# Kernel optimization log

Measured on AMD Instinct MI355X. Metric: run time of the kernel, lower is better.

The kernel has to match this reference:

```python
import jax, jax.numpy as jnp
import numpy as np

N_NODES = 87381  # complete 4-ary tree of depth 9: (4**9 - 1) / 3
VOCAB = 32000
D_IN = 256
M_DIM = 256


def setup_inputs() -> dict:
    key = jax.random.key(0)
    ks = jax.random.split(key, 10)
    w = lambda k, s: jax.random.normal(k, s, dtype=jnp.float32) * 0.05
    return {
        "tokens": jax.random.randint(ks[0], (N_NODES,), 0, VOCAB),
        "branching": 4,
        "emb": w(ks[1], (VOCAB, D_IN)),
        "Wioux": w(ks[2], (D_IN, 3 * M_DIM)),
        "bioux": w(ks[3], (3 * M_DIM,)),
        "Wiouh": w(ks[4], (M_DIM, 3 * M_DIM)),
        "biouh": w(ks[5], (3 * M_DIM,)),
        "Wfx": w(ks[6], (D_IN, M_DIM)),
        "bfx": w(ks[7], (M_DIM,)),
        "Wfh": w(ks[8], (M_DIM, M_DIM)),
        "bfh": w(ks[9], (M_DIM,)),
    }


def _levels(n, b):
    # BFS level boundaries (start, size) for a complete b-ary tree with n nodes
    out, start, size = [], 0, 1
    while start < n:
        out.append((start, min(size, n - start)))
        start += size
        size *= b
    return out


def reference(tokens, branching, emb, Wioux, bioux, Wiouh, biouh, Wfx, bfx, Wfh, bfh):
    N = tokens.shape[0]
    b = int(branching)
    M = Wfh.shape[0]
    x = emb[tokens]                       # [N, D_IN] per-node inputs
    xiou = x @ Wioux + bioux              # [N, 3M] precomputed input gate terms
    xf = x @ Wfx + bfx                    # [N, M]
    h = jnp.zeros((N, M), x.dtype)
    c = jnp.zeros((N, M), x.dtype)
    for (s, sz) in reversed(_levels(N, b)):  # leaves -> root
        idx = jnp.arange(s, s + sz)
        child = idx[:, None] * b + 1 + jnp.arange(b)[None, :]   # [sz, b]
        valid = (child < N)[..., None].astype(x.dtype)          # [sz, b, 1]
        ci = jnp.where(child < N, child, 0)
        ch = h[ci] * valid                                      # [sz, b, M]
        cc = c[ci] * valid
        iou = xiou[idx] + ch.sum(axis=1) @ Wiouh + biouh        # [sz, 3M]
        i, o, u = jnp.split(iou, 3, axis=1)
        i, o, u = jax.nn.sigmoid(i), jax.nn.sigmoid(o), jnp.tanh(u)
        f = jax.nn.sigmoid(ch @ Wfh + bfh + xf[idx][:, None, :])  # [sz, b, M]
        c_new = i * u + jnp.sum(f * cc * valid, axis=1)
        h_new = o * jnp.tanh(c_new)
        c = c.at[idx].set(c_new)
        h = h.at[idx].set(h_new)
    return h  # hidden state of every node; root state is h[0]
```

## Files before the change

kernel.cpp:

```cpp
#include <hip/hip_runtime.h>
#include <cstdint>
#include <cstddef>

typedef _Float16 f16;
typedef __attribute__((ext_vector_type(8))) _Float16 half8;
typedef __attribute__((ext_vector_type(4))) _Float16 half4;
typedef __attribute__((ext_vector_type(8))) short short8;
typedef __attribute__((ext_vector_type(4))) float floatx4;
typedef __attribute__((ext_vector_type(8))) float floatx8;

__device__ __forceinline__ float rcp_(float x) { return __builtin_amdgcn_rcpf(x); }
__device__ __forceinline__ float sigm(float x) { return rcp_(1.f + __expf(-x)); }
__device__ __forceinline__ float tanh_(float x) { return 1.f - 2.f * rcp_(1.f + __expf(2.f * x)); }

__device__ __forceinline__ short8 ld16_coh(const void* p) {
  unsigned long long lo = __hip_atomic_load((const unsigned long long*)p,
      __ATOMIC_RELAXED, __HIP_MEMORY_SCOPE_AGENT);
  unsigned long long hi = __hip_atomic_load((const unsigned long long*)p + 1,
      __ATOMIC_RELAXED, __HIP_MEMORY_SCOPE_AGENT);
  union { unsigned long long u[2]; short8 s; } v;
  v.u[0] = lo; v.u[1] = hi;
  return v.s;
}
__device__ __forceinline__ void st2_coh(f16* p, f16 x) {
  __hip_atomic_store((unsigned short*)p, __builtin_bit_cast(unsigned short, x),
                     __ATOMIC_RELAXED, __HIP_MEMORY_SCOPE_AGENT);
}

__global__ __launch_bounds__(256) void gemm128d(
    const f16* __restrict__ A0, const f16* __restrict__ B0, f16* __restrict__ C0,
    int ldc0, int nt0, int tiles0,
    const f16* __restrict__ A1, const f16* __restrict__ B1, f16* __restrict__ C1,
    int ldc1, int nt1)
{
  const f16* A; const f16* BT; f16* C; int ldc_, mi, ni;
  int bid = blockIdx.x;
  bid = (bid & 7) * ((int)gridDim.x >> 3) + (bid >> 3);
  if (bid < tiles0) { A = A0; BT = B0; C = C0; ldc_ = ldc0; mi = bid / nt0; ni = bid % nt0; }
  else { int r = bid - tiles0; A = A1; BT = B1; C = C1; ldc_ = ldc1; mi = r / nt1; ni = r % nt1; }
  const int m0 = mi * 128;
  const int n0 = ni * 128;

  __shared__ short lA[128 * 72];
  __shared__ short lB[128 * 72];
  const int t = threadIdx.x;
  const int wave = t >> 6;
  const int lane = t & 63;
  const int ln = lane & 15;
  const int quad = lane >> 4;
  const int wr = wave >> 1;
  const int wc = wave & 1;

  floatx4 acc[4][4];
#pragma unroll
  for (int i = 0; i < 4; ++i)
#pragma unroll
    for (int j = 0; j < 4; ++j) acc[i][j] = (floatx4){0.f, 0.f, 0.f, 0.f};

#pragma unroll
  for (int st = 0; st < 4; ++st) {
    const int k0 = st * 64;
#pragma unroll
    for (int i = 0; i < 4; ++i) {
      int chunk = t + 256 * i;
      int row = chunk >> 3;
      int cc = chunk & 7;
      *(short8*)&lA[row * 72 + cc * 8] =
          *(const short8*)(A + (size_t)(m0 + row) * 256 + k0 + cc * 8);
      *(short8*)&lB[row * 72 + cc * 8] =
          *(const short8*)(BT + (size_t)(n0 + row) * 256 + k0 + cc * 8);
    }
    __syncthreads();
#pragma unroll
    for (int ks = 0; ks < 2; ++ks) {
      const int kk = ks * 32 + quad * 8;
      half8 a[4], b[4];
#pragma unroll
      for (int rf = 0; rf < 4; ++rf)
        a[rf] = __builtin_bit_cast(half8,
            *(const short8*)&lA[(wr * 64 + rf * 16 + ln) * 72 + kk]);
#pragma unroll
      for (int cf = 0; cf < 4; ++cf)
        b[cf] = __builtin_bit_cast(half8,
            *(const short8*)&lB[(wc * 64 + cf * 16 + ln) * 72 + kk]);
#pragma unroll
      for (int rf = 0; rf < 4; ++rf)
#pragma unroll
        for (int cf = 0; cf < 4; ++cf)
          acc[rf][cf] = __builtin_amdgcn_mfma_f32_16x16x32_f16(
              a[rf], b[cf], acc[rf][cf], 0, 0, 0);
    }
    __syncthreads();
  }
#pragma unroll
  for (int rf = 0; rf < 4; ++rf)
#pragma unroll
    for (int cf = 0; cf < 4; ++cf)
#pragma unroll
      for (int r = 0; r < 4; ++r) {
        int row = m0 + wr * 64 + rf * 16 + quad * 4 + r;
        int col = n0 + wc * 64 + cf * 16 + ln;
        C[(size_t)row * ldc_ + col] = (f16)acc[rf][cf][r];
      }
}

__global__ __launch_bounds__(256) void prep(
    const float* __restrict__ emb, const float* __restrict__ Wioux,
    const float* __restrict__ Wfx, const float* __restrict__ Wiouh,
    const float* __restrict__ Wfh,
    f16* __restrict__ emb_h, f16* __restrict__ BTX,
    f16* __restrict__ WiouhT, f16* __restrict__ WfhT,
    int* __restrict__ ctr)
{
  int idx = blockIdx.x * 256 + threadIdx.x;
  if (idx < 8) ctr[idx] = 0;
  if (idx < 2048000) {
    floatx4 v = *(const floatx4*)(emb + 4 * (size_t)idx);
    half4 o;
#pragma unroll
    for (int j = 0; j < 4; ++j) o[j] = (f16)v[j];
    *(half4*)(emb_h + 4 * (size_t)idx) = o;
  } else if (idx < 2310144) {
    int r = idx - 2048000;
    int j = r >> 8, k = r & 255;
    BTX[r] = (f16)((j < 768) ? Wioux[(size_t)k * 768 + j]
                             : Wfx[(size_t)k * 256 + (j - 768)]);
  } else if (idx < 2506752) {
    int r = idx - 2310144;
    int j = r >> 8, k = r & 255;
    WiouhT[r] = (f16)Wiouh[(size_t)k * 768 + j];
  } else {
    int r = idx - 2506752;
    int j = r >> 8, k = r & 255;
    WfhT[r] = (f16)Wfh[(size_t)k * 256 + j];
  }
}

__global__ __launch_bounds__(256) void elem8(
    const int* __restrict__ tokens, const f16* __restrict__ TIOUF,
    const float* __restrict__ bioux, const float* __restrict__ biouh,
    f16* __restrict__ c16, float* __restrict__ h, f16* __restrict__ h16,
    f16* __restrict__ hsum16, int s, int sz, int s_up, int sz_up)
{
  __shared__ float hsh[8 * 260];
  const int t = threadIdx.x;
  const int nloc = t >> 5;
  const int d0 = (t & 31) * 8;
  const int base = s + 8 * blockIdx.x;
  const int node = base + nloc;
  const int lim = s + sz;

  if (node < lim) {
    const f16* ti = TIOUF + (size_t)tokens[node] * 1024;
    half8 t0 = *(const half8*)(ti + d0);
    half8 t1 = *(const half8*)(ti + 256 + d0);
    half8 t2 = *(const half8*)(ti + 512 + d0);
    floatx8 bi0 = *(const floatx8*)(bioux + d0) + *(const floatx8*)(biouh + d0);
    floatx8 bi1 = *(const floatx8*)(bioux + 256 + d0) + *(const floatx8*)(biouh + 256 + d0);
    floatx8 bi2 = *(const floatx8*)(bioux + 512 + d0) + *(const floatx8*)(biouh + 512 + d0);

    float cv[8];
#pragma unroll
    for (int j = 0; j < 8; ++j)
      cv[j] = sigm((float)t0[j] + bi0[j]) * tanh_((float)t2[j] + bi2[j]);

    half8 c8, h8;
    floatx8 hf;
#pragma unroll
    for (int j = 0; j < 8; ++j) {
      float hv = sigm((float)t1[j] + bi1[j]) * tanh_(cv[j]);
      c8[j] = (f16)cv[j];
      h8[j] = (f16)hv;
      hf[j] = hv;
    }
    *(half8*)(c16 + (size_t)node * 256 + d0) = c8;
    *(floatx8*)(h + (size_t)node * 256 + d0) = hf;
    *(half8*)(h16 + (size_t)node * 256 + d0) = h8;
    *(floatx8*)&hsh[nloc * 260 + d0] = hf;
  }
  __syncthreads();

  if (t < 64) {
    int p = t >> 5;
    int dd = (t & 31) * 8;
    int parent = ((base - 1) >> 2) + p;
    if (parent < s_up + sz_up) {
      floatx8 v = *(const floatx8*)&hsh[(4 * p + 0) * 260 + dd] +
                  *(const floatx8*)&hsh[(4 * p + 1) * 260 + dd] +
                  *(const floatx8*)&hsh[(4 * p + 2) * 260 + dd] +
                  *(const floatx8*)&hsh[(4 * p + 3) * 260 + dd];
      half8 o;
#pragma unroll
      for (int j = 0; j < 8; ++j) o[j] = (f16)v[j];
      *(half8*)(hsum16 + (size_t)(parent - s_up) * 256 + dd) = o;
    }
  }
}

template <bool COH>
__device__ __forceinline__ void do_tile(
    short* lA, short* lC,
    const int* __restrict__ tokens, const f16* __restrict__ TIOUF,
    const f16* __restrict__ WiouhT, const f16* __restrict__ WfhT,
    const float* __restrict__ bioux, const float* __restrict__ biouh,
    const float* __restrict__ bfx, const float* __restrict__ bfh,
    f16* __restrict__ c16, float* __restrict__ h, f16* __restrict__ h16,
    const f16* __restrict__ hsum_in, f16* __restrict__ hsum_out,
    int s, int sz, int sz_up, int pt, int pg)
{
  const int t = threadIdx.x;
  const int p0 = s + pt * 16;
  const int c0 = 4 * p0 + 1;

#pragma unroll
  for (int i = 0; i < 5; ++i) {
    int chunk = t + 512 * i;
    int row = chunk >> 5;
    int cc = chunk & 31;
    const f16* src = (row < 16)
        ? hsum_in + (size_t)(pt * 16 + row) * 256 + cc * 8
        : h16 + (size_t)(c0 + row - 16) * 256 + cc * 8;
    short8 v;
    if constexpr (COH) v = ld16_coh(src); else v = *(const short8*)src;
    *(short8*)&lA[row * 256 + (cc ^ (row & 7)) * 8] = v;
  }
  if constexpr (COH) {
#pragma unroll
    for (int i = 0; i < 2; ++i) {
      int chunk = t + 512 * i;
      int row = chunk >> 4;
      int cc = chunk & 15;
      short8 v = ld16_coh(c16 + (size_t)(c0 + row) * 256 + pg * 128 + cc * 8);
      *(short8*)&lC[row * 136 + cc * 8] = v;
    }
  }
  __syncthreads();

  const int wave = t >> 6;
  const int lane = t & 63;
  const int ln = lane & 15;
  const int q = lane >> 4;
  const int rb = ln & 7;
  const int dim = (pg * 8 + wave) * 16 + ln;
  const int dl = wave * 16 + ln;

  floatx4 accI[3], accF[4];
#pragma unroll
  for (int i = 0; i < 3; ++i) accI[i] = (floatx4){0.f, 0.f, 0.f, 0.f};
#pragma unroll
  for (int i = 0; i < 4; ++i) accF[i] = (floatx4){0.f, 0.f, 0.f, 0.f};

  const short* aBase = &lA[ln * 256];
  const f16* b0p = WiouhT + (size_t)dim * 256 + 8 * q;
  const f16* b1p = b0p + 256 * 256;
  const f16* b2p = b0p + 512 * 256;
  const f16* bfp = WfhT + (size_t)dim * 256 + 8 * q;

#pragma unroll
  for (int ks = 0; ks < 8; ++ks) {
    const int ko = 32 * ks;
    const int co = ((q + 4 * ks) ^ rb) * 8;
    half8 ah = __builtin_bit_cast(half8, *(const short8*)(aBase + co));
    half8 b0 = *(const half8*)(b0p + ko);
    half8 b1 = *(const half8*)(b1p + ko);
    half8 b2 = *(const half8*)(b2p + ko);
    half8 bf = *(const half8*)(bfp + ko);
    accI[0] = __builtin_amdgcn_mfma_f32_16x16x32_f16(ah, b0, accI[0], 0, 0, 0);
    accI[1] = __builtin_amdgcn_mfma_f32_16x16x32_f16(ah, b1, accI[1], 0, 0, 0);
    accI[2] = __builtin_amdgcn_mfma_f32_16x16x32_f16(ah, b2, accI[2], 0, 0, 0);
#pragma unroll
    for (int rt = 0; rt < 4; ++rt) {
      half8 ac = __builtin_bit_cast(half8,
          *(const short8*)(aBase + (16 + 16 * rt) * 256 + co));
      accF[rt] = __builtin_amdgcn_mfma_f32_16x16x32_f16(ac, bf, accF[rt], 0, 0, 0);
    }
  }
  __syncthreads();

  float* myFS = (float*)lA + wave * (16 * 17);

  const float bi0 = bioux[dim] + biouh[dim];
  const float bi1 = bioux[256 + dim] + biouh[256 + dim];
  const float bi2 = bioux[512 + dim] + biouh[512 + dim];
  const float bff = bfx[dim] + bfh[dim];

#pragma unroll
  for (int rt = 0; rt < 4; ++rt) {
    int po = 4 * rt + q;
    int tok = tokens[p0 + po];
    float xff = (float)TIOUF[(size_t)tok * 1024 + 768 + dim] + bff;
    float fs = 0.f;
#pragma unroll
    for (int r = 0; r < 4; ++r) {
      float ccv;
      if constexpr (COH)
        ccv = (float)__builtin_bit_cast(f16, lC[(16 * rt + 4 * q + r) * 136 + dl]);
      else
        ccv = (float)c16[(size_t)(c0 + 16 * rt + 4 * q + r) * 256 + dim];
      fs += sigm(accF[rt][r] + xff) * ccv;
    }
    myFS[po * 17 + ln] = fs;
  }
  asm volatile("s_waitcnt lgkmcnt(0)" ::: "memory");
  __builtin_amdgcn_sched_barrier(0);

  const int szrem = sz - pt * 16;
  float hsum = 0.f;
#pragma unroll
  for (int r = 0; r < 4; ++r) {
    int po = 4 * q + r;
    const f16* tp = TIOUF + (size_t)tokens[p0 + po] * 1024;
    float iv = sigm(accI[0][r] + (float)tp[dim] + bi0);
    float ov = sigm(accI[1][r] + (float)tp[256 + dim] + bi1);
    float uv = tanh_(accI[2][r] + (float)tp[512 + dim] + bi2);
    float cn = iv * uv + myFS[po * 17 + ln];
    float hn = ov * tanh_(cn);
    hsum += hn;
    if (po < szrem) {
      size_t pi = (size_t)(p0 + po);
      if constexpr (COH) {
        st2_coh(c16 + pi * 256 + dim, (f16)cn);
        st2_coh(h16 + pi * 256 + dim, (f16)hn);
      } else {
        c16[pi * 256 + dim] = (f16)cn;
        h16[pi * 256 + dim] = (f16)hn;
      }
      h[pi * 256 + dim] = hn;
    }
  }
  if (sz_up > 0) {
    int g_row = 4 * pt + q;
    if (g_row < sz_up) {
      if constexpr (COH)
        st2_coh(hsum_out + (size_t)g_row * 256 + dim, (f16)hsum);
      else
        hsum_out[(size_t)g_row * 256 + dim] = (f16)hsum;
    }
  }
}

__global__ __launch_bounds__(512, 8) void fused_level(
    const int* __restrict__ tokens, const f16* __restrict__ TIOUF,
    const f16* __restrict__ WiouhT, const f16* __restrict__ WfhT,
    const float* __restrict__ bioux, const float* __restrict__ biouh,
    const float* __restrict__ bfx, const float* __restrict__ bfh,
    f16* __restrict__ c16, float* __restrict__ h, f16* __restrict__ h16,
    const f16* __restrict__ hsum_in, f16* __restrict__ hsum_out,
    int s, int sz, int sz_up)
{
  __shared__ short lA[80 * 256];
  int b = blockIdx.x;
  int lb = (b & 7) * ((int)gridDim.x >> 3) + (b >> 3);
  do_tile<false>(lA, nullptr, tokens, TIOUF, WiouhT, WfhT, bioux, biouh,
                 bfx, bfh, c16, h, h16, hsum_in, hsum_out, s, sz, sz_up,
                 lb >> 1, lb & 1);
}

__global__ __launch_bounds__(512, 4) void tail3(
    const int* __restrict__ tokens, const f16* __restrict__ TIOUF,
    const f16* __restrict__ WiouhT, const f16* __restrict__ WfhT,
    const float* __restrict__ bioux, const float* __restrict__ biouh,
    const float* __restrict__ bfx, const float* __restrict__ bfh,
    f16* __restrict__ c16, float* __restrict__ h, f16* __restrict__ h16,
    f16* __restrict__ hsumA, f16* __restrict__ hsumB, int* __restrict__ ctr)
{
  __shared__ short lA[80 * 256];
  __shared__ short lC[64 * 136];
  const int pg = blockIdx.x;
#pragma unroll 1
  for (int l = 0; l < 3; ++l) {
    const int s  = (l == 0) ? 5 : (l == 1) ? 1 : 0;
    const int sz = (l == 0) ? 16 : (l == 1) ? 4 : 1;
    const int up = (l == 0) ? 4 : (l == 1) ? 1 : 0;
    const f16* hin = (l == 1) ? hsumA : hsumB;
    f16* hout = (l == 0) ? hsumA : (l == 1) ? hsumB : nullptr;
    __syncthreads();
    do_tile<true>(lA, lC, tokens, TIOUF, WiouhT, WfhT, bioux, biouh,
                  bfx, bfh, c16, h, h16, hin, hout, s, sz, up, 0, pg);
    if (l < 2) {
      asm volatile("s_waitcnt vmcnt(0)" ::: "memory");
      __syncthreads();
      if (threadIdx.x == 0) {
        __hip_atomic_fetch_add(&ctr[l], 1, __ATOMIC_RELAXED,
                               __HIP_MEMORY_SCOPE_AGENT);
        while (__hip_atomic_load(&ctr[l], __ATOMIC_RELAXED,
                                 __HIP_MEMORY_SCOPE_AGENT) < 2)
          __builtin_amdgcn_s_sleep(1);
      }
      __syncthreads();
    }
  }
}

extern "C" void kernel_launch(void* const* d_in, const int* in_sizes, int n_in,
                              void* d_out, int out_size, void* d_ws, size_t ws_size,
                              hipStream_t stream) {
  const int*   tokens = (const int*)d_in[0];
  const float* emb    = (const float*)d_in[2];
  const float* Wioux  = (const float*)d_in[3];
  const float* bioux  = (const float*)d_in[4];
  const float* Wiouh  = (const float*)d_in[5];
  const float* biouh  = (const float*)d_in[6];
  const float* Wfx    = (const float*)d_in[7];
  const float* bfx    = (const float*)d_in[8];
  const float* Wfh    = (const float*)d_in[9];
  const float* bfh    = (const float*)d_in[10];
  float* h = (float*)d_out;
  (void)in_sizes; (void)n_in; (void)out_size; (void)ws_size;

  f16* emb_h   = (f16*)d_ws;
  f16* BTX     = emb_h   + 8192000;
  f16* WiouhT  = BTX     + 262144;
  f16* WfhT    = WiouhT  + 196608;
  f16* TIOUF   = WfhT    + 65536;
  f16* hsumB   = TIOUF   + (size_t)32768000;
  f16* FH_dead = hsumB   + (size_t)12582912;
  f16* h16     = FH_dead + (size_t)22396928;
  f16* hsumA   = h16     + (size_t)22396928;
  f16* c16     = hsumA   + (size_t)4194304;
  int* ctr     = (int*)FH_dead;

  prep<<<10049, 256, 0, stream>>>(emb, Wioux, Wfx, Wiouh, Wfh,
                                  emb_h, BTX, WiouhT, WfhT, ctr);

  gemm128d<<<2000, 256, 0, stream>>>(emb_h, BTX, TIOUF, 1024, 8, 2000,
                                     emb_h, BTX, TIOUF, 1024, 8);

  elem8<<<8192, 256, 0, stream>>>(tokens, TIOUF, bioux, biouh,
                                  c16, h, h16, hsumA, 21845, 65536, 5461, 16384);

  const int LV[5][3] = {{5461, 16384, 4096}, {1365, 4096, 1024},
                        {341, 1024, 256},    {85, 256, 64}, {21, 64, 16}};
  for (int i = 0; i < 5; ++i) {
    int s = LV[i][0], sz = LV[i][1], up = LV[i][2];
    const f16* hin = (i & 1) ? hsumB : hsumA;
    f16* hout = (i & 1) ? hsumA : hsumB;
    int blocks = 2 * ((sz + 15) / 16);
    fused_level<<<blocks, 512, 0, stream>>>(
        tokens, TIOUF, WiouhT, WfhT, bioux, biouh, bfx, bfh,
        c16, h, h16, hin, hout, s, sz, up);
  }

  tail3<<<2, 512, 0, stream>>>(
      tokens, TIOUF, WiouhT, WfhT, bioux, biouh, bfx, bfh,
      c16, h, h16, hsumA, hsumB, ctr);
}
```

Before: 415.9 us.

## Process 32 parents per block in fused level kernel to reuse weight fragments

The per-level tile function is templated on the parents-per-tile count. The fused level kernel now handles 32 parents per block instead of 16, so each weight fragment loaded from global memory feeds two M-subtiles of MFMAs, which roughly halves weight traffic per parent. The price is double the LDS per block, more accumulator registers and a lower occupancy bound. The grid is also halved, which leaves the small upper levels with very few blocks; the launch count assumes each level size divides by 32.

```diff
diff --git a/kernel.cpp b/kernel.cpp
--- a/kernel.cpp
+++ b/kernel.cpp
@@ -197,7 +197,7 @@
   }
 }
 
-template <bool COH>
+template <bool COH, int PP>
 __device__ __forceinline__ void do_tile(
     short* lA, short* lC,
     const int* __restrict__ tokens, const f16* __restrict__ TIOUF,
@@ -209,24 +209,27 @@
     int s, int sz, int sz_up, int pt, int pg)
 {
   const int t = threadIdx.x;
-  const int p0 = s + pt * 16;
+  const int p0 = s + pt * PP;
   const int c0 = 4 * p0 + 1;
-
-#pragma unroll
-  for (int i = 0; i < 5; ++i) {
+  constexpr int ROWS = 5 * PP;
+  constexpr int MI = PP / 16;
+  constexpr int NF = PP / 4;
+
+#pragma unroll
+  for (int i = 0; i < ROWS / 16; ++i) {
     int chunk = t + 512 * i;
     int row = chunk >> 5;
     int cc = chunk & 31;
-    const f16* src = (row < 16)
-        ? hsum_in + (size_t)(pt * 16 + row) * 256 + cc * 8
-        : h16 + (size_t)(c0 + row - 16) * 256 + cc * 8;
+    const f16* src = (row < PP)
+        ? hsum_in + (size_t)(pt * PP + row) * 256 + cc * 8
+        : h16 + (size_t)(c0 + row - PP) * 256 + cc * 8;
     short8 v;
     if constexpr (COH) v = ld16_coh(src); else v = *(const short8*)src;
     *(short8*)&lA[row * 256 + (cc ^ (row & 7)) * 8] = v;
   }
   if constexpr (COH) {
 #pragma unroll
-    for (int i = 0; i < 2; ++i) {
+    for (int i = 0; i < PP / 8; ++i) {
       int chunk = t + 512 * i;
       int row = chunk >> 4;
       int cc = chunk & 15;
@@ -244,11 +247,14 @@
   const int dim = (pg * 8 + wave) * 16 + ln;
   const int dl = wave * 16 + ln;
 
-  floatx4 accI[3], accF[4];
-#pragma unroll
-  for (int i = 0; i < 3; ++i) accI[i] = (floatx4){0.f, 0.f, 0.f, 0.f};
-#pragma unroll
-  for (int i = 0; i < 4; ++i) accF[i] = (floatx4){0.f, 0.f, 0.f, 0.f};
+  floatx4 accI[3][MI];
+  floatx4 accF[NF];
+#pragma unroll
+  for (int i = 0; i < 3; ++i)
+#pragma unroll
+    for (int m = 0; m < MI; ++m) accI[i][m] = (floatx4){0.f, 0.f, 0.f, 0.f};
+#pragma unroll
+  for (int i = 0; i < NF; ++i) accF[i] = (floatx4){0.f, 0.f, 0.f, 0.f};
 
   const short* aBase = &lA[ln * 256];
   const f16* b0p = WiouhT + (size_t)dim * 256 + 8 * q;
@@ -260,24 +266,28 @@
   for (int ks = 0; ks < 8; ++ks) {
     const int ko = 32 * ks;
     const int co = ((q + 4 * ks) ^ rb) * 8;
-    half8 ah = __builtin_bit_cast(half8, *(const short8*)(aBase + co));
     half8 b0 = *(const half8*)(b0p + ko);
     half8 b1 = *(const half8*)(b1p + ko);
     half8 b2 = *(const half8*)(b2p + ko);
     half8 bf = *(const half8*)(bfp + ko);
-    accI[0] = __builtin_amdgcn_mfma_f32_16x16x32_f16(ah, b0, accI[0], 0, 0, 0);
-    accI[1] = __builtin_amdgcn_mfma_f32_16x16x32_f16(ah, b1, accI[1], 0, 0, 0);
-    accI[2] = __builtin_amdgcn_mfma_f32_16x16x32_f16(ah, b2, accI[2], 0, 0, 0);
-#pragma unroll
-    for (int rt = 0; rt < 4; ++rt) {
+#pragma unroll
+    for (int m = 0; m < MI; ++m) {
+      half8 ah = __builtin_bit_cast(half8,
+          *(const short8*)(aBase + m * 16 * 256 + co));
+      accI[0][m] = __builtin_amdgcn_mfma_f32_16x16x32_f16(ah, b0, accI[0][m], 0, 0, 0);
+      accI[1][m] = __builtin_amdgcn_mfma_f32_16x16x32_f16(ah, b1, accI[1][m], 0, 0, 0);
+      accI[2][m] = __builtin_amdgcn_mfma_f32_16x16x32_f16(ah, b2, accI[2][m], 0, 0, 0);
+    }
+#pragma unroll
+    for (int fi = 0; fi < NF; ++fi) {
       half8 ac = __builtin_bit_cast(half8,
-          *(const short8*)(aBase + (16 + 16 * rt) * 256 + co));
-      accF[rt] = __builtin_amdgcn_mfma_f32_16x16x32_f16(ac, bf, accF[rt], 0, 0, 0);
+          *(const short8*)(aBase + (PP + 16 * fi) * 256 + co));
+      accF[fi] = __builtin_amdgcn_mfma_f32_16x16x32_f16(ac, bf, accF[fi], 0, 0, 0);
     }
   }
   __syncthreads();
 
-  float* myFS = (float*)lA + wave * (16 * 17);
+  float* myFS = (float*)lA + wave * (PP * 17);
 
   const float bi0 = bioux[dim] + biouh[dim];
   const float bi1 = bioux[256 + dim] + biouh[256 + dim];
@@ -285,8 +295,8 @@
   const float bff = bfx[dim] + bfh[dim];
 
 #pragma unroll
-  for (int rt = 0; rt < 4; ++rt) {
-    int po = 4 * rt + q;
+  for (int fi = 0; fi < NF; ++fi) {
+    int po = 4 * fi + q;
     int tok = tokens[p0 + po];
     float xff = (float)TIOUF[(size_t)tok * 1024 + 768 + dim] + bff;
     float fs = 0.f;
@@ -294,52 +304,55 @@
     for (int r = 0; r < 4; ++r) {
       float ccv;
       if constexpr (COH)
-        ccv = (float)__builtin_bit_cast(f16, lC[(16 * rt + 4 * q + r) * 136 + dl]);
+        ccv = (float)__builtin_bit_cast(f16, lC[(16 * fi + 4 * q + r) * 136 + dl]);
       else
-        ccv = (float)c16[(size_t)(c0 + 16 * rt + 4 * q + r) * 256 + dim];
-      fs += sigm(accF[rt][r] + xff) * ccv;
+        ccv = (float)c16[(size_t)(c0 + 16 * fi + 4 * q + r) * 256 + dim];
+      fs += sigm(accF[fi][r] + xff) * ccv;
     }
     myFS[po * 17 + ln] = fs;
   }
   asm volatile("s_waitcnt lgkmcnt(0)" ::: "memory");
   __builtin_amdgcn_sched_barrier(0);
 
-  const int szrem = sz - pt * 16;
-  float hsum = 0.f;
-#pragma unroll
-  for (int r = 0; r < 4; ++r) {
-    int po = 4 * q + r;
-    const f16* tp = TIOUF + (size_t)tokens[p0 + po] * 1024;
-    float iv = sigm(accI[0][r] + (float)tp[dim] + bi0);
-    float ov = sigm(accI[1][r] + (float)tp[256 + dim] + bi1);
-    float uv = tanh_(accI[2][r] + (float)tp[512 + dim] + bi2);
-    float cn = iv * uv + myFS[po * 17 + ln];
-    float hn = ov * tanh_(cn);
-    hsum += hn;
-    if (po < szrem) {
-      size_t pi = (size_t)(p0 + po);
-      if constexpr (COH) {
-        st2_coh(c16 + pi * 256 + dim, (f16)cn);
-        st2_coh(h16 + pi * 256 + dim, (f16)hn);
-      } else {
-        c16[pi * 256 + dim] = (f16)cn;
-        h16[pi * 256 + dim] = (f16)hn;
+  const int szrem = sz - pt * PP;
+#pragma unroll
+  for (int m = 0; m < MI; ++m) {
+    float hsum = 0.f;
+#pragma unroll
+    for (int r = 0; r < 4; ++r) {
+      int po = m * 16 + 4 * q + r;
+      const f16* tp = TIOUF + (size_t)tokens[p0 + po] * 1024;
+      float iv = sigm(accI[0][m][r] + (float)tp[dim] + bi0);
+      float ov = sigm(accI[1][m][r] + (float)tp[256 + dim] + bi1);
+      float uv = tanh_(accI[2][m][r] + (float)tp[512 + dim] + bi2);
+      float cn = iv * uv + myFS[po * 17 + ln];
+      float hn = ov * tanh_(cn);
+      hsum += hn;
+      if (po < szrem) {
+        size_t pi = (size_t)(p0 + po);
+        if constexpr (COH) {
+          st2_coh(c16 + pi * 256 + dim, (f16)cn);
+          st2_coh(h16 + pi * 256 + dim, (f16)hn);
+        } else {
+          c16[pi * 256 + dim] = (f16)cn;
+          h16[pi * 256 + dim] = (f16)hn;
+        }
+        h[pi * 256 + dim] = hn;
       }
-      h[pi * 256 + dim] = hn;
-    }
-  }
-  if (sz_up > 0) {
-    int g_row = 4 * pt + q;
-    if (g_row < sz_up) {
-      if constexpr (COH)
-        st2_coh(hsum_out + (size_t)g_row * 256 + dim, (f16)hsum);
-      else
-        hsum_out[(size_t)g_row * 256 + dim] = (f16)hsum;
-    }
-  }
-}
-
-__global__ __launch_bounds__(512, 8) void fused_level(
+    }
+    if (sz_up > 0) {
+      int g_row = (PP / 4) * pt + 4 * m + q;
+      if (g_row < sz_up) {
+        if constexpr (COH)
+          st2_coh(hsum_out + (size_t)g_row * 256 + dim, (f16)hsum);
+        else
+          hsum_out[(size_t)g_row * 256 + dim] = (f16)hsum;
+      }
+    }
+  }
+}
+
+__global__ __launch_bounds__(512, 4) void fused_level(
     const int* __restrict__ tokens, const f16* __restrict__ TIOUF,
     const f16* __restrict__ WiouhT, const f16* __restrict__ WfhT,
     const float* __restrict__ bioux, const float* __restrict__ biouh,
@@ -348,12 +361,13 @@
     const f16* __restrict__ hsum_in, f16* __restrict__ hsum_out,
     int s, int sz, int sz_up)
 {
-  __shared__ short lA[80 * 256];
+  __shared__ short lA[160 * 256];
   int b = blockIdx.x;
-  int lb = (b & 7) * ((int)gridDim.x >> 3) + (b >> 3);
-  do_tile<false>(lA, nullptr, tokens, TIOUF, WiouhT, WfhT, bioux, biouh,
-                 bfx, bfh, c16, h, h16, hsum_in, hsum_out, s, sz, sz_up,
-                 lb >> 1, lb & 1);
+  int lb = ((int)gridDim.x & 7) ? b
+         : (b & 7) * ((int)gridDim.x >> 3) + (b >> 3);
+  do_tile<false, 32>(lA, nullptr, tokens, TIOUF, WiouhT, WfhT, bioux, biouh,
+                     bfx, bfh, c16, h, h16, hsum_in, hsum_out, s, sz, sz_up,
+                     lb >> 1, lb & 1);
 }
 
 __global__ __launch_bounds__(512, 4) void tail3(
@@ -375,8 +389,8 @@
     const f16* hin = (l == 1) ? hsumA : hsumB;
     f16* hout = (l == 0) ? hsumA : (l == 1) ? hsumB : nullptr;
     __syncthreads();
-    do_tile<true>(lA, lC, tokens, TIOUF, WiouhT, WfhT, bioux, biouh,
-                  bfx, bfh, c16, h, h16, hin, hout, s, sz, up, 0, pg);
+    do_tile<true, 16>(lA, lC, tokens, TIOUF, WiouhT, WfhT, bioux, biouh,
+                      bfx, bfh, c16, h, h16, hin, hout, s, sz, up, 0, pg);
     if (l < 2) {
       asm volatile("s_waitcnt vmcnt(0)" ::: "memory");
       __syncthreads();
@@ -435,7 +449,7 @@
     int s = LV[i][0], sz = LV[i][1], up = LV[i][2];
     const f16* hin = (i & 1) ? hsumB : hsumA;
     f16* hout = (i & 1) ? hsumA : hsumB;
-    int blocks = 2 * ((sz + 15) / 16);
+    int blocks = 2 * (sz / 32);
     fused_level<<<blocks, 512, 0, stream>>>(
         tokens, TIOUF, WiouhT, WfhT, bioux, biouh, bfx, bfh,
         c16, h, h16, hin, hout, s, sz, up);
```

Result: no change. 420.1 us (+1.0%).
